# Kernel tuning notes

Measured on AMD Instinct MI355X. Metric: run time of the kernel, lower is better.

The kernel has to match this reference:

```python
import jax, jax.numpy as jnp
import numpy as np

TAU = 2.0      # LIFNode default tau
VTH = 1.0      # v_threshold
ALPHA = 2.0    # ATan surrogate alpha
EPS = 1e-5     # BatchNorm eps
SCALE = 0.125  # hardcoded attention scale
HEADS = 8

@jax.custom_vjp
def atan_spike(x):
    return (x >= 0.0).astype(x.dtype)

def _atan_fwd(x):
    return atan_spike(x), x

def _atan_bwd(x, g):
    sg = (ALPHA / 2.0) / (1.0 + (jnp.pi / 2.0 * ALPHA * x) ** 2)
    return (g * sg,)

atan_spike.defvjp(_atan_fwd, _atan_bwd)

def lif(x_seq):
    # multi-step LIF: v' = v + (x - v)/tau ; spike = H(v'-1) ; hard reset to 0 (detach_reset)
    def step(v, x):
        v = v + (x - v) / TAU
        s = atan_spike(v - VTH)
        v = v * (1.0 - jax.lax.stop_gradient(s))
        return v, s
    _, spikes = jax.lax.scan(step, jnp.zeros_like(x_seq[0]), x_seq)
    return spikes

def bn(x, gamma, beta, mean, var):
    # inference-mode BatchNorm1d over channel axis 2 of [T,B,C,N]
    inv = gamma / jnp.sqrt(var + EPS)
    return x * inv[None, None, :, None] + (beta - mean * inv)[None, None, :, None]

def setup_inputs() -> dict:
    key = jax.random.key(0)
    ks = jax.random.split(key, 24)
    T, B, C, H, W = 4, 8, 512, 32, 32
    inp = {"x": jax.random.normal(ks[0], (T, B, C, H, W), dtype=jnp.float32)}
    i = 1
    for p in ("q", "k", "v", "proj"):
        inp[p + "_w"] = jax.random.normal(ks[i], (C, C), dtype=jnp.float32) / np.sqrt(C); i += 1
        inp[p + "_gamma"] = jax.random.uniform(ks[i], (C,), minval=0.5, maxval=1.5, dtype=jnp.float32); i += 1
        inp[p + "_beta"] = 0.1 * jax.random.normal(ks[i], (C,), dtype=jnp.float32); i += 1
        inp[p + "_mean"] = 0.1 * jax.random.normal(ks[i], (C,), dtype=jnp.float32); i += 1
        inp[p + "_var"] = jax.random.uniform(ks[i], (C,), minval=0.5, maxval=1.5, dtype=jnp.float32); i += 1
    inp["proj_b"] = 0.1 * jax.random.normal(ks[i], (C,), dtype=jnp.float32)
    return inp

def reference(x, q_w, q_gamma, q_beta, q_mean, q_var,
              k_w, k_gamma, k_beta, k_mean, k_var,
              v_w, v_gamma, v_beta, v_mean, v_var,
              proj_w, proj_gamma, proj_beta, proj_mean, proj_var, proj_b):
    T, B, C, H, W = x.shape
    N = H * W
    d = C // HEADS
    s = lif(x).reshape(T, B, C, N)  # proj_lif then flatten HW

    def branch(w, g, b, m, v_):
        y = jnp.einsum('oc,tbcn->tbon', w, s)  # conv1x1 == channel GEMM
        y = lif(bn(y, g, b, m, v_))
        # [T,B,C,N] -> [T,B,h,N,d]
        return y.reshape(T, B, HEADS, d, N).transpose(0, 1, 2, 4, 3)

    q = branch(q_w, q_gamma, q_beta, q_mean, q_var)
    k = branch(k_w, k_gamma, k_beta, k_mean, k_var)
    v = branch(v_w, v_gamma, v_beta, v_mean, v_var)

    kv = jnp.einsum('tbhnd,tbhne->tbhde', k, v)          # k^T v : [T,B,h,d,d]
    att = jnp.einsum('tbhnd,tbhde->tbhne', q, kv) * SCALE  # [T,B,h,N,d]
    att = att.transpose(0, 1, 2, 4, 3).reshape(T, B, C, N)
    a = lif(att)

    y = jnp.einsum('oc,tbcn->tbon', proj_w, a) + proj_b[None, None, :, None]
    y = bn(y, proj_gamma, proj_beta, proj_mean, proj_var)
    return y.reshape(T, B, C, H, W)
```

## Files before the change

kernel.cpp:

```cpp
#include <hip/hip_runtime.h>
#include <cstdint>
#include <cstddef>

typedef unsigned short u16;
typedef __attribute__((ext_vector_type(8))) short sh8;
typedef __attribute__((ext_vector_type(8))) _Float16 hf8;
typedef __attribute__((ext_vector_type(4))) float f4;

#define MFMA16B(a, b, c) __builtin_amdgcn_mfma_f32_16x16x32_bf16((a), (b), (c), 0, 0, 0)
#define MFMA16H(a, b, c) __builtin_amdgcn_mfma_f32_16x16x32_f16((a), (b), (c), 0, 0, 0)

__device__ __forceinline__ u16 f2bf(float f) {
  union { float f; uint32_t u; } v; v.f = f;
  uint32_t u = v.u;
  uint32_t lsb = (u >> 16) & 1u;
  return (u16)((u + 0x7fffu + lsb) >> 16);
}
__device__ __forceinline__ float bf2f(u16 h) {
  union { uint32_t u; float f; } v; v.u = ((uint32_t)h) << 16;
  return v.f;
}

__device__ __forceinline__ void aload16(const void* g, void* l) {
  __builtin_amdgcn_global_load_lds(
      (const __attribute__((address_space(1))) uint32_t*)g,
      (__attribute__((address_space(3))) uint32_t*)l, 16, 0, 0);
}

#define MFMA12(Af, Bf, NB)                                                    \
  {                                                                           \
    __builtin_amdgcn_s_setprio(1);                                            \
    _Pragma("unroll") for (int nf = 0; nf < 2; ++nf)                          \
      _Pragma("unroll") for (int mf = 0; mf < 6; ++mf)                        \
        acc[mf][(NB) + nf] = MFMA16H(Af[mf], Bf[nf], acc[mf][(NB) + nf]);     \
    __builtin_amdgcn_s_setprio(0);                                            \
  }

#define MFMA8(Af, Bf, NB)                                                     \
  {                                                                           \
    __builtin_amdgcn_s_setprio(1);                                            \
    _Pragma("unroll") for (int nf = 0; nf < 2; ++nf)                          \
      _Pragma("unroll") for (int mf = 0; mf < 4; ++mf)                        \
        acc[mf][(NB) + nf] = MFMA16H(Af[mf], Bf[nf], acc[mf][(NB) + nf]);     \
    __builtin_amdgcn_s_setprio(0);                                            \
  }

__global__ void prep_weights(const float* __restrict__ qw, const float* __restrict__ kw,
                             const float* __restrict__ vw, const float* __restrict__ pw,
                             u16* __restrict__ w2qkv, u16* __restrict__ w2p) {
  #pragma clang fp contract(off)
  int row = blockIdx.x;
  for (int c = threadIdx.x; c < 512; c += 256) {
    const float* src;
    if (row < 1536) {
      int br = row >> 9;
      src = (br == 0 ? qw : (br == 1 ? kw : vw)) + (size_t)(row & 511) * 512;
    } else {
      src = pw + (size_t)(row - 1536) * 512;
    }
    float w = src[c];
    _Float16 h0 = (_Float16)w;
    float r1 = w - (float)h0;
    _Float16 h1 = (_Float16)r1;
    union { _Float16 h; u16 u; } u0, u1;
    u0.h = h0; u1.h = h1;
    if (row < 1536) {
      w2qkv[(size_t)row * 1024 + c] = u0.u;
      w2qkv[(size_t)row * 1024 + 512 + c] = u1.u;
    } else {
      int m = row - 1536;
      w2p[(size_t)m * 1024 + c] = u0.u;
      w2p[(size_t)m * 1024 + 512 + c] = u1.u;
    }
  }
}

__global__ void bn_prep(const float* __restrict__ g0, const float* __restrict__ b0,
                        const float* __restrict__ m0, const float* __restrict__ v0,
                        const float* __restrict__ g1, const float* __restrict__ b1,
                        const float* __restrict__ m1, const float* __restrict__ v1,
                        const float* __restrict__ g2, const float* __restrict__ b2,
                        const float* __restrict__ m2, const float* __restrict__ v2,
                        const float* __restrict__ g3, const float* __restrict__ b3,
                        const float* __restrict__ m3, const float* __restrict__ v3,
                        float* __restrict__ inv, float* __restrict__ add) {
  #pragma clang fp contract(off)
  int s = blockIdx.x >> 1;
  int i = (blockIdx.x & 1) * 256 + threadIdx.x;
  const float* g  = s == 0 ? g0 : s == 1 ? g1 : s == 2 ? g2 : g3;
  const float* be = s == 0 ? b0 : s == 1 ? b1 : s == 2 ? b2 : b3;
  const float* mu = s == 0 ? m0 : s == 1 ? m1 : s == 2 ? m2 : m3;
  const float* va = s == 0 ? v0 : s == 1 ? v1 : s == 2 ? v2 : v3;
  float iv = g[i] / sqrtf(va[i] + 1e-5f);
  inv[s * 512 + i] = iv;
  add[s * 512 + i] = be[i] - mu[i] * iv;
}

__global__ __launch_bounds__(256) void lif0(const float* __restrict__ x, u16* __restrict__ sT) {
  #pragma clang fp contract(off)
  __shared__ u16 st[64 * 80];
  const int tid = threadIdx.x;
  const int n0 = blockIdx.x * 64;
  const int c0 = blockIdx.y * 64;
  const int b = blockIdx.z;
  const int cl = tid >> 2;
  const int ns = (tid & 3) * 16;
  const int nr = tid >> 2;
  const int cs = (tid & 3) * 16;
  float vv[16];
#pragma unroll
  for (int i = 0; i < 16; i++) vv[i] = 0.f;
  for (int t = 0; t < 4; ++t) {
    const float* xp = x + ((size_t)((t * 8 + b) * 512 + c0 + cl)) * 1024 + n0 + ns;
#pragma unroll
    for (int q = 0; q < 4; ++q) {
      f4 xv = *(const f4*)(xp + q * 4);
#pragma unroll
      for (int j = 0; j < 4; ++j) {
        int i = q * 4 + j;
        float v2 = vv[i] + (xv[j] - vv[i]) * 0.5f;
        int spk = (v2 - 1.0f >= 0.0f);
        st[(ns + i) * 80 + cl] = spk ? (u16)0x3C00 : (u16)0;
        vv[i] = spk ? 0.0f : v2;
      }
    }
    __syncthreads();
    u16* gp = sT + ((size_t)((t * 8 + b) * 1024 + n0 + nr)) * 512 + c0 + cs;
    *(sh8*)(gp) = *(const sh8*)&st[nr * 80 + cs];
    *(sh8*)(gp + 8) = *(const sh8*)&st[nr * 80 + cs + 8];
    __syncthreads();
  }
}

__global__ __launch_bounds__(512, 2) void qkv_gemm(
    const u16* __restrict__ w2,
    const u16* __restrict__ sT,
    const float* __restrict__ inv4, const float* __restrict__ add4,
    u16* __restrict__ qs, u16* __restrict__ ks, u16* __restrict__ vs) {
  #pragma clang fp contract(off)
  __shared__ u16 lA[2][192 * 64];
  __shared__ u16 lB[3][256 * 64];
  const int tid = threadIdx.x;
  const int bid = blockIdx.x;
  const int orig = (bid & 7) * 32 + (bid >> 3);
  const int mI = orig & 7;
  const int nI = (orig >> 3) & 3;
  const int b  = orig >> 5;
  const int m0 = mI * 192;
  const int n0 = nI * 256;
  const int wid = tid >> 6, lane = tid & 63;
  const int l15 = lane & 15, l4 = lane >> 4;
  const int wm = wid >> 2, wn = wid & 3;
  const int swz = l15 & 7;
  const int srow = tid >> 3;
  const int ss = (tid & 7) ^ (srow & 7);
  int aoff[3];
#pragma unroll
  for (int c = 0; c < 3; ++c)
    aoff[c] = (m0 + c * 64 + srow) * 1024 + (ss >> 2) * 512 + (ss & 3) * 8;
  int boff[4];
#pragma unroll
  for (int c = 0; c < 4; ++c)
    boff[c] = (n0 + c * 64 + srow) * 512 + (ss >> 2) * 32 + (ss & 3) * 8;

  auto stA = [&](int ii) {
    int k0 = (ii & 15) * 32;
    u16* d = &lA[ii & 1][0];
#pragma unroll
    for (int c = 0; c < 3; ++c)
      aload16(w2 + (size_t)(aoff[c] + k0), d + c * 4096 + tid * 8);
  };
  auto stB = [&](int P) {
    int k0 = (P & 7) * 64;
    const u16* bb = sT + (size_t)(P >> 3) * 4194304 + (size_t)b * 524288;
    u16* d = &lB[P % 3][0];
#pragma unroll
    for (int c = 0; c < 4; ++c)
      aload16(bb + (size_t)(boff[c] + k0), d + c * 4096 + tid * 8);
  };

  const f4 fz = {0.f, 0.f, 0.f, 0.f};
  f4 acc[6][4];
  f4 vst[6][4];
#pragma unroll
  for (int i = 0; i < 6; i++)
#pragma unroll
    for (int j = 0; j < 4; j++) vst[i][j] = fz;

  stA(0); stB(0); stB(1);
  asm volatile("s_waitcnt vmcnt(4)" ::: "memory");
  __builtin_amdgcn_s_barrier();
  __builtin_amdgcn_sched_barrier(0);

  for (int t = 0; t < 4; ++t) {
#pragma unroll
    for (int i = 0; i < 6; i++)
#pragma unroll
      for (int j = 0; j < 4; j++) acc[i][j] = fz;

    for (int i = 0; i < 16; ++i) {
      const int ii = t * 16 + i;
      const int P = ii >> 1;
      const u16* bufA = &lA[ii & 1][0];
      const u16* bufB = &lB[P % 3][0];
      const int sb = (ii & 1) * 4;
      const bool issueB = ((ii & 1) == 0) && (P + 2 < 32);
      if (ii < 63) stA(ii + 1);
      if (issueB) stB(P + 2);
      hf8 A0[6], Bq[2];
#pragma unroll
      for (int mf = 0; mf < 6; ++mf) {
        int r = wm * 96 + mf * 16 + l15;
        A0[mf] = *(const hf8*)&bufA[r * 64 + ((l4 ^ swz) * 8)];
      }
#pragma unroll
      for (int nf = 0; nf < 2; ++nf) {
        int r = wn * 64 + nf * 16 + l15;
        Bq[nf] = *(const hf8*)&bufB[r * 64 + (((sb + l4) ^ swz) * 8)];
      }
      MFMA12(A0, Bq, 0);
      hf8 B1[2];
#pragma unroll
      for (int nf = 0; nf < 2; ++nf) {
        int r = wn * 64 + (2 + nf) * 16 + l15;
        B1[nf] = *(const hf8*)&bufB[r * 64 + (((sb + l4) ^ swz) * 8)];
      }
      MFMA12(A0, B1, 2);
      hf8 A1[6];
#pragma unroll
      for (int mf = 0; mf < 6; ++mf) {
        int r = wm * 96 + mf * 16 + l15;
        A1[mf] = *(const hf8*)&bufA[r * 64 + (((4 + l4) ^ swz) * 8)];
      }
      MFMA12(A1, B1, 2);
      MFMA12(A1, Bq, 0);
      if (((ii & 1) == 0) && issueB) {
        asm volatile("s_waitcnt vmcnt(4)" ::: "memory");
      } else {
        asm volatile("s_waitcnt vmcnt(0)" ::: "memory");
      }
      __builtin_amdgcn_s_barrier();
      __builtin_amdgcn_sched_barrier(0);
    }
#pragma unroll
    for (int mf = 0; mf < 6; ++mf) {
      int f0 = m0 + wm * 96 + mf * 16;
      int br = f0 >> 9;
      u16* dst = br == 0 ? qs : (br == 1 ? ks : vs);
      int ocb = f0 & 511;
#pragma unroll
      for (int r = 0; r < 4; ++r) {
        int oc = ocb + l4 * 4 + r;
        float iv = inv4[br * 512 + oc];
        float ad = add4[br * 512 + oc];
        size_t rowbase = ((size_t)((t * 8 + b) * 512 + oc)) * 1024 + n0;
#pragma unroll
        for (int nf = 0; nf < 4; ++nf) {
          float z = acc[mf][nf][r] * iv + ad;
          float v2 = vst[mf][nf][r];
          v2 = v2 + (z - v2) * 0.5f;
          int spk = (v2 - 1.0f >= 0.0f);
          vst[mf][nf][r] = spk ? 0.0f : v2;
          dst[rowbase + wn * 64 + nf * 16 + l15] = spk ? (u16)0x3F80 : (u16)0;
        }
      }
    }
  }
}

__global__ __launch_bounds__(256) void kv_gemm(const u16* __restrict__ ks,
                                               const u16* __restrict__ vs,
                                               float* __restrict__ kvp) {
  const int tbh = blockIdx.x;
  const int tid = threadIdx.x;
  const int wv = tid >> 6, lane = tid & 63, l15 = lane & 15, l4 = lane >> 4;
  const size_t cb = ((size_t)(tbh >> 3) * 512 + (size_t)(tbh & 7) * 64) * 1024;
  const u16* vbase = vs + cb;
  const u16* kbase = ks + cb;
  const f4 fz = {0.f, 0.f, 0.f, 0.f};
  f4 acc[4];
#pragma unroll
  for (int i = 0; i < 4; i++) acc[i] = fz;
  for (int s = 0; s < 32; ++s) {
    int kk = s * 32 + l4 * 8;
    sh8 av = *(const sh8*)(vbase + (size_t)(wv * 16 + l15) * 1024 + kk);
#pragma unroll
    for (int df = 0; df < 4; ++df) {
      sh8 bk = *(const sh8*)(kbase + (size_t)(df * 16 + l15) * 1024 + kk);
      acc[df] = MFMA16B(av, bk, acc[df]);
    }
  }
  float* out = kvp + (size_t)tbh * 4096;
#pragma unroll
  for (int df = 0; df < 4; ++df)
#pragma unroll
    for (int r = 0; r < 4; ++r)
      out[(wv * 16 + l4 * 4 + r) * 64 + df * 16 + l15] = acc[df][r];
}

__global__ __launch_bounds__(256) void att_lif(const u16* __restrict__ qs,
                                               const float* __restrict__ kvp,
                                               u16* __restrict__ aT) {
  #pragma clang fp contract(off)
  __shared__ u16 ldsb[64 * 72 * 2 + 128 * 72];
  u16* lkhi = ldsb;
  u16* lklo = ldsb + 64 * 72;
  u16* lqT = ldsb + 64 * 72 * 2;
  u16* lsp = ldsb;
  const int tid = threadIdx.x;
  const int n0 = blockIdx.x * 128;
  const int b = blockIdx.y >> 3;
  const int h = blockIdx.y & 7;
  const int wv = tid >> 6, lane = tid & 63, l15 = lane & 15, l4 = lane >> 4;
  const int e_s = tid >> 2, ds_ = (tid & 3) * 16;
  const f4 fz = {0.f, 0.f, 0.f, 0.f};
  f4 vst[4][2];
#pragma unroll
  for (int i = 0; i < 4; i++)
#pragma unroll
    for (int j = 0; j < 2; j++) vst[i][j] = fz;

  for (int t = 0; t < 4; ++t) {
    int tb = t * 8 + b;
    int tbh = tb * 8 + h;
    {
      const float* base = kvp + (size_t)tbh * 4096 + e_s * 64 + ds_;
#pragma unroll
      for (int q = 0; q < 4; ++q) {
        f4 s4 = *(const f4*)(base + q * 4);
#pragma unroll
        for (int j = 0; j < 4; ++j) {
          float sv = s4[j];
          u16 hb = f2bf(sv);
          float lof = sv - bf2f(hb);
          lkhi[e_s * 72 + ds_ + q * 4 + j] = hb;
          lklo[e_s * 72 + ds_ + q * 4 + j] = f2bf(lof);
        }
      }
    }
    {
      const u16* qb = qs + ((size_t)tb * 512 + h * 64) * 1024 + n0;
#pragma unroll
      for (int it = 0; it < 4; ++it) {
        int lin = it * 2048 + tid * 8;
        int d = lin >> 7, j0 = lin & 127;
        sh8 qv = *(const sh8*)(qb + (size_t)d * 1024 + j0);
#pragma unroll
        for (int j = 0; j < 8; ++j) lqT[(j0 + j) * 72 + d] = (u16)qv[j];
      }
    }
    __syncthreads();
    f4 acc[4][2];
#pragma unroll
    for (int i = 0; i < 4; i++)
#pragma unroll
      for (int j = 0; j < 2; j++) acc[i][j] = fz;
#pragma unroll
    for (int ksx = 0; ksx < 2; ++ksx) {
      sh8 bq[2];
#pragma unroll
      for (int nf = 0; nf < 2; ++nf)
        bq[nf] = *(const sh8*)&lqT[(wv * 32 + nf * 16 + l15) * 72 + ksx * 32 + l4 * 8];
#pragma unroll
      for (int mf = 0; mf < 4; ++mf) {
        sh8 ah = *(const sh8*)&lkhi[(mf * 16 + l15) * 72 + ksx * 32 + l4 * 8];
        sh8 al = *(const sh8*)&lklo[(mf * 16 + l15) * 72 + ksx * 32 + l4 * 8];
#pragma unroll
        for (int nf = 0; nf < 2; ++nf) {
          acc[mf][nf] = MFMA16B(ah, bq[nf], acc[mf][nf]);
          acc[mf][nf] = MFMA16B(al, bq[nf], acc[mf][nf]);
        }
      }
    }
    __syncthreads();
#pragma unroll
    for (int mf = 0; mf < 4; ++mf)
#pragma unroll
      for (int nf = 0; nf < 2; ++nf)
#pragma unroll
        for (int r = 0; r < 4; ++r) {
          float xatt = acc[mf][nf][r] * 0.125f;
          float v2 = vst[mf][nf][r];
          v2 = v2 + (xatt - v2) * 0.5f;
          int spk = (v2 - 1.0f >= 0.0f);
          vst[mf][nf][r] = spk ? 0.0f : v2;
          int e = mf * 16 + l4 * 4 + r;
          int n = wv * 32 + nf * 16 + l15;
          lsp[n * 72 + e] = spk ? (u16)0x3C00 : (u16)0;
        }
    __syncthreads();
    {
#pragma unroll
      for (int it = 0; it < 2; ++it) {
        int lin = it * 256 + tid;
        int n = lin >> 2, es = (lin & 3) * 16;
        u16* gp = aT + ((size_t)(tb * 1024 + n0 + n)) * 512 + h * 64 + es;
        *(sh8*)gp = *(const sh8*)&lsp[n * 72 + es];
        *(sh8*)(gp + 8) = *(const sh8*)&lsp[n * 72 + es + 8];
      }
    }
    __syncthreads();
  }
}

__global__ __launch_bounds__(512, 2) void proj_gemm(
    const u16* __restrict__ w2,
    const u16* __restrict__ aT,
    const float* __restrict__ inv4, const float* __restrict__ add4,
    const float* __restrict__ pb, float* __restrict__ out) {
  #pragma clang fp contract(off)
  __shared__ u16 lA[2][128 * 64];
  __shared__ u16 lB[3][256 * 64];
  const int tid = threadIdx.x;
  const int bid = blockIdx.x;
  const int orig = (bid & 7) * 64 + (bid >> 3);
  const int mI = orig & 3;
  const int nI = (orig >> 2) & 3;
  const int tb = orig >> 4;
  const int m0 = mI * 128;
  const int n0 = nI * 256;
  const int wid = tid >> 6, lane = tid & 63;
  const int l15 = lane & 15, l4 = lane >> 4;
  const int wm = wid >> 2, wn = wid & 3;
  const int swz = l15 & 7;
  const int srow = tid >> 3;
  const int ss = (tid & 7) ^ (srow & 7);
  int aoff[2];
#pragma unroll
  for (int c = 0; c < 2; ++c)
    aoff[c] = (m0 + c * 64 + srow) * 1024 + (ss >> 2) * 512 + (ss & 3) * 8;
  int boff[4];
#pragma unroll
  for (int c = 0; c < 4; ++c)
    boff[c] = (n0 + c * 64 + srow) * 512 + (ss >> 2) * 32 + (ss & 3) * 8;
  const u16* bb = aT + (size_t)tb * 524288;

  auto stA = [&](int ii) {
    int k0 = (ii & 15) * 32;
    u16* d = &lA[ii & 1][0];
#pragma unroll
    for (int c = 0; c < 2; ++c)
      aload16(w2 + (size_t)(aoff[c] + k0), d + c * 4096 + tid * 8);
  };
  auto stB = [&](int P) {
    int k0 = (P & 7) * 64;
    u16* d = &lB[P % 3][0];
#pragma unroll
    for (int c = 0; c < 4; ++c)
      aload16(bb + (size_t)(boff[c] + k0), d + c * 4096 + tid * 8);
  };

  const f4 fz = {0.f, 0.f, 0.f, 0.f};
  f4 acc[4][4];
#pragma unroll
  for (int i = 0; i < 4; i++)
#pragma unroll
    for (int j = 0; j < 4; j++) acc[i][j] = fz;

  stA(0); stB(0); stB(1);
  asm volatile("s_waitcnt vmcnt(4)" ::: "memory");
  __builtin_amdgcn_s_barrier();
  __builtin_amdgcn_sched_barrier(0);

  for (int ii = 0; ii < 16; ++ii) {
    const int P = ii >> 1;
    const u16* bufA = &lA[ii & 1][0];
    const u16* bufB = &lB[P % 3][0];
    const int sb = (ii & 1) * 4;
    const bool issueB = ((ii & 1) == 0) && (P + 2 < 8);
    if (ii < 15) stA(ii + 1);
    if (issueB) stB(P + 2);
    hf8 A0[4], Bq[2];
#pragma unroll
    for (int mf = 0; mf < 4; ++mf) {
      int r = wm * 64 + mf * 16 + l15;
      A0[mf] = *(const hf8*)&bufA[r * 64 + ((l4 ^ swz) * 8)];
    }
#pragma unroll
    for (int nf = 0; nf < 2; ++nf) {
      int r = wn * 64 + nf * 16 + l15;
      Bq[nf] = *(const hf8*)&bufB[r * 64 + (((sb + l4) ^ swz) * 8)];
    }
    MFMA8(A0, Bq, 0);
    hf8 B1[2];
#pragma unroll
    for (int nf = 0; nf < 2; ++nf) {
      int r = wn * 64 + (2 + nf) * 16 + l15;
      B1[nf] = *(const hf8*)&bufB[r * 64 + (((sb + l4) ^ swz) * 8)];
    }
    MFMA8(A0, B1, 2);
    hf8 A1[4];
#pragma unroll
    for (int mf = 0; mf < 4; ++mf) {
      int r = wm * 64 + mf * 16 + l15;
      A1[mf] = *(const hf8*)&bufA[r * 64 + (((4 + l4) ^ swz) * 8)];
    }
    MFMA8(A1, B1, 2);
    MFMA8(A1, Bq, 0);
    if (((ii & 1) == 0) && issueB) {
      asm volatile("s_waitcnt vmcnt(4)" ::: "memory");
    } else {
      asm volatile("s_waitcnt vmcnt(0)" ::: "memory");
    }
    __builtin_amdgcn_s_barrier();
    __builtin_amdgcn_sched_barrier(0);
  }
#pragma unroll
  for (int mf = 0; mf < 4; ++mf) {
#pragma unroll
    for (int r = 0; r < 4; ++r) {
      int o = m0 + wm * 64 + mf * 16 + l4 * 4 + r;
      float iv = inv4[3 * 512 + o];
      float ad = add4[3 * 512 + o];
      float bias = pb[o];
      size_t rowbase = ((size_t)(tb * 512 + o)) * 1024 + n0;
#pragma unroll
      for (int nf = 0; nf < 4; ++nf) {
        float z = (acc[mf][nf][r] + bias) * iv + ad;
        out[rowbase + wn * 64 + nf * 16 + l15] = z;
      }
    }
  }
}

extern "C" void kernel_launch(void* const* d_in, const int* in_sizes, int n_in,
                              void* d_out, int out_size, void* d_ws, size_t ws_size,
                              hipStream_t stream) {
  const float* x = (const float*)d_in[0];
  const float* qw = (const float*)d_in[1];
  const float* kw = (const float*)d_in[6];
  const float* vw = (const float*)d_in[11];
  const float* pw = (const float*)d_in[16];
  const float* pb = (const float*)d_in[21];

  char* p = (char*)d_ws;
  u16* w2qkv = (u16*)p; p += (size_t)1536 * 1024 * 2;
  u16* w2p = (u16*)p;   p += (size_t)512 * 1024 * 2;
  float* inv4 = (float*)p; p += 4 * 512 * 4;
  float* add4 = (float*)p; p += 4 * 512 * 4;
  u16* sT = (u16*)p;    p += (size_t)4 * 8 * 1024 * 512 * 2;
  u16* qs = (u16*)p;    p += (size_t)4 * 8 * 512 * 1024 * 2;
  u16* ks = (u16*)p;    p += (size_t)4 * 8 * 512 * 1024 * 2;
  u16* vs = (u16*)p;    p += (size_t)4 * 8 * 512 * 1024 * 2;
  float* kvp = (float*)p; p += (size_t)256 * 4096 * 4;
  u16* aT = sT;
  float* out = (float*)d_out;

  prep_weights<<<dim3(2048), dim3(256), 0, stream>>>(qw, kw, vw, pw, w2qkv, w2p);
  bn_prep<<<dim3(8), dim3(256), 0, stream>>>(
      (const float*)d_in[2], (const float*)d_in[3], (const float*)d_in[4], (const float*)d_in[5],
      (const float*)d_in[7], (const float*)d_in[8], (const float*)d_in[9], (const float*)d_in[10],
      (const float*)d_in[12], (const float*)d_in[13], (const float*)d_in[14], (const float*)d_in[15],
      (const float*)d_in[17], (const float*)d_in[18], (const float*)d_in[19], (const float*)d_in[20],
      inv4, add4);
  lif0<<<dim3(16, 8, 8), dim3(256), 0, stream>>>(x, sT);
  qkv_gemm<<<dim3(256), dim3(512), 0, stream>>>(w2qkv, sT, inv4, add4, qs, ks, vs);
  kv_gemm<<<dim3(256), dim3(256), 0, stream>>>(ks, vs, kvp);
  att_lif<<<dim3(8, 64), dim3(256), 0, stream>>>(qs, kvp, aT);
  proj_gemm<<<dim3(512), dim3(512), 0, stream>>>(w2p, aT, inv4, add4, pb, out);
}
```

Baseline: 258.5 us.

## Shrink GEMM tiles to 64-row blocks for higher occupancy in qkv and proj

Both the qkv and projection GEMMs move from large M tiles (192/128 rows) with a triple-buffered B and staggered waits to 64-row M tiles with double-buffered A and B at K step 32. Launch bounds rise to four blocks per CU and grid sizes grow to 768 and 1024 blocks. The aim is more resident waves and better CU coverage so latency is hidden by occupancy instead of deep software pipelining. In exchange each block gets less operand reuse, the same weights and activations are fetched from global memory more often, and every K step now waits on all outstanding loads with vmcnt(0).

```diff
diff --git a/kernel.cpp b/kernel.cpp
--- a/kernel.cpp
+++ b/kernel.cpp
@@ -26,24 +26,6 @@
       (const __attribute__((address_space(1))) uint32_t*)g,
       (__attribute__((address_space(3))) uint32_t*)l, 16, 0, 0);
 }
-
-#define MFMA12(Af, Bf, NB)                                                    \
-  {                                                                           \
-    __builtin_amdgcn_s_setprio(1);                                            \
-    _Pragma("unroll") for (int nf = 0; nf < 2; ++nf)                          \
-      _Pragma("unroll") for (int mf = 0; mf < 6; ++mf)                        \
-        acc[mf][(NB) + nf] = MFMA16H(Af[mf], Bf[nf], acc[mf][(NB) + nf]);     \
-    __builtin_amdgcn_s_setprio(0);                                            \
-  }
-
-#define MFMA8(Af, Bf, NB)                                                     \
-  {                                                                           \
-    __builtin_amdgcn_s_setprio(1);                                            \
-    _Pragma("unroll") for (int nf = 0; nf < 2; ++nf)                          \
-      _Pragma("unroll") for (int mf = 0; mf < 4; ++mf)                        \
-        acc[mf][(NB) + nf] = MFMA16H(Af[mf], Bf[nf], acc[mf][(NB) + nf]);     \
-    __builtin_amdgcn_s_setprio(0);                                            \
-  }
 
 __global__ void prep_weights(const float* __restrict__ qw, const float* __restrict__ kw,
                              const float* __restrict__ vw, const float* __restrict__ pw,
@@ -132,119 +114,104 @@
   }
 }
 
-__global__ __launch_bounds__(512, 2) void qkv_gemm(
+__global__ __launch_bounds__(512, 4) void qkv_gemm(
     const u16* __restrict__ w2,
     const u16* __restrict__ sT,
     const float* __restrict__ inv4, const float* __restrict__ add4,
     u16* __restrict__ qs, u16* __restrict__ ks, u16* __restrict__ vs) {
   #pragma clang fp contract(off)
-  __shared__ u16 lA[2][192 * 64];
-  __shared__ u16 lB[3][256 * 64];
+  __shared__ u16 lA[2][64 * 64];
+  __shared__ u16 lB[2][256 * 32];
   const int tid = threadIdx.x;
   const int bid = blockIdx.x;
-  const int orig = (bid & 7) * 32 + (bid >> 3);
-  const int mI = orig & 7;
-  const int nI = (orig >> 3) & 3;
-  const int b  = orig >> 5;
-  const int m0 = mI * 192;
+  const int orig = (bid & 7) * 96 + (bid >> 3);
+  const int mI = orig % 24;
+  const int rest = orig / 24;
+  const int nI = rest & 3;
+  const int b  = rest >> 2;
+  const int m0 = mI * 64;
   const int n0 = nI * 256;
   const int wid = tid >> 6, lane = tid & 63;
   const int l15 = lane & 15, l4 = lane >> 4;
   const int wm = wid >> 2, wn = wid & 3;
-  const int swz = l15 & 7;
-  const int srow = tid >> 3;
-  const int ss = (tid & 7) ^ (srow & 7);
-  int aoff[3];
-#pragma unroll
-  for (int c = 0; c < 3; ++c)
-    aoff[c] = (m0 + c * 64 + srow) * 1024 + (ss >> 2) * 512 + (ss & 3) * 8;
-  int boff[4];
-#pragma unroll
-  for (int c = 0; c < 4; ++c)
-    boff[c] = (n0 + c * 64 + srow) * 512 + (ss >> 2) * 32 + (ss & 3) * 8;
+  const int swzA = l15 & 7;
+  const int swzB = l15 & 3;
+  const int ssA = (tid & 7) ^ ((tid >> 3) & 7);
+  const int aoff = (m0 + (tid >> 3)) * 1024 + (ssA >> 2) * 512 + (ssA & 3) * 8;
+  const int ssB = (tid & 3) ^ ((tid >> 2) & 3);
+  int boff[2];
+#pragma unroll
+  for (int c = 0; c < 2; ++c)
+    boff[c] = (n0 + c * 128 + (tid >> 2)) * 512 + ssB * 8;
 
   auto stA = [&](int ii) {
     int k0 = (ii & 15) * 32;
-    u16* d = &lA[ii & 1][0];
-#pragma unroll
-    for (int c = 0; c < 3; ++c)
-      aload16(w2 + (size_t)(aoff[c] + k0), d + c * 4096 + tid * 8);
+    aload16(w2 + (size_t)(aoff + k0), &lA[ii & 1][tid * 8]);
   };
-  auto stB = [&](int P) {
-    int k0 = (P & 7) * 64;
-    const u16* bb = sT + (size_t)(P >> 3) * 4194304 + (size_t)b * 524288;
-    u16* d = &lB[P % 3][0];
-#pragma unroll
-    for (int c = 0; c < 4; ++c)
+  auto stB = [&](int ii) {
+    int k0 = (ii & 15) * 32;
+    const u16* bb = sT + (size_t)(ii >> 4) * 4194304 + (size_t)b * 524288;
+    u16* d = &lB[ii & 1][0];
+#pragma unroll
+    for (int c = 0; c < 2; ++c)
       aload16(bb + (size_t)(boff[c] + k0), d + c * 4096 + tid * 8);
   };
 
   const f4 fz = {0.f, 0.f, 0.f, 0.f};
-  f4 acc[6][4];
-  f4 vst[6][4];
-#pragma unroll
-  for (int i = 0; i < 6; i++)
+  f4 acc[2][4];
+  f4 vst[2][4];
+#pragma unroll
+  for (int i = 0; i < 2; i++)
 #pragma unroll
     for (int j = 0; j < 4; j++) vst[i][j] = fz;
 
-  stA(0); stB(0); stB(1);
-  asm volatile("s_waitcnt vmcnt(4)" ::: "memory");
+  stA(0); stB(0);
+  asm volatile("s_waitcnt vmcnt(0)" ::: "memory");
   __builtin_amdgcn_s_barrier();
   __builtin_amdgcn_sched_barrier(0);
 
   for (int t = 0; t < 4; ++t) {
 #pragma unroll
-    for (int i = 0; i < 6; i++)
+    for (int i = 0; i < 2; i++)
 #pragma unroll
       for (int j = 0; j < 4; j++) acc[i][j] = fz;
 
     for (int i = 0; i < 16; ++i) {
       const int ii = t * 16 + i;
-      const int P = ii >> 1;
       const u16* bufA = &lA[ii & 1][0];
-      const u16* bufB = &lB[P % 3][0];
-      const int sb = (ii & 1) * 4;
-      const bool issueB = ((ii & 1) == 0) && (P + 2 < 32);
-      if (ii < 63) stA(ii + 1);
-      if (issueB) stB(P + 2);
-      hf8 A0[6], Bq[2];
-#pragma unroll
-      for (int mf = 0; mf < 6; ++mf) {
-        int r = wm * 96 + mf * 16 + l15;
-        A0[mf] = *(const hf8*)&bufA[r * 64 + ((l4 ^ swz) * 8)];
-      }
-#pragma unroll
-      for (int nf = 0; nf < 2; ++nf) {
+      const u16* bufB = &lB[ii & 1][0];
+      if (ii < 63) { stA(ii + 1); stB(ii + 1); }
+      hf8 A0[2], A1[2], Bf[4];
+#pragma unroll
+      for (int mf = 0; mf < 2; ++mf) {
+        int r = wm * 32 + mf * 16 + l15;
+        A0[mf] = *(const hf8*)&bufA[r * 64 + (((l4) ^ swzA) * 8)];
+        A1[mf] = *(const hf8*)&bufA[r * 64 + (((4 + l4) ^ swzA) * 8)];
+      }
+#pragma unroll
+      for (int nf = 0; nf < 4; ++nf) {
         int r = wn * 64 + nf * 16 + l15;
-        Bq[nf] = *(const hf8*)&bufB[r * 64 + (((sb + l4) ^ swz) * 8)];
-      }
-      MFMA12(A0, Bq, 0);
-      hf8 B1[2];
-#pragma unroll
-      for (int nf = 0; nf < 2; ++nf) {
-        int r = wn * 64 + (2 + nf) * 16 + l15;
-        B1[nf] = *(const hf8*)&bufB[r * 64 + (((sb + l4) ^ swz) * 8)];
-      }
-      MFMA12(A0, B1, 2);
-      hf8 A1[6];
-#pragma unroll
-      for (int mf = 0; mf < 6; ++mf) {
-        int r = wm * 96 + mf * 16 + l15;
-        A1[mf] = *(const hf8*)&bufA[r * 64 + (((4 + l4) ^ swz) * 8)];
-      }
-      MFMA12(A1, B1, 2);
-      MFMA12(A1, Bq, 0);
-      if (((ii & 1) == 0) && issueB) {
-        asm volatile("s_waitcnt vmcnt(4)" ::: "memory");
-      } else {
-        asm volatile("s_waitcnt vmcnt(0)" ::: "memory");
-      }
+        Bf[nf] = *(const hf8*)&bufB[r * 32 + ((l4 ^ swzB) * 8)];
+      }
+      __builtin_amdgcn_s_setprio(1);
+#pragma unroll
+      for (int nf = 0; nf < 4; ++nf)
+#pragma unroll
+        for (int mf = 0; mf < 2; ++mf)
+          acc[mf][nf] = MFMA16H(A0[mf], Bf[nf], acc[mf][nf]);
+#pragma unroll
+      for (int nf = 0; nf < 4; ++nf)
+#pragma unroll
+        for (int mf = 0; mf < 2; ++mf)
+          acc[mf][nf] = MFMA16H(A1[mf], Bf[nf], acc[mf][nf]);
+      __builtin_amdgcn_s_setprio(0);
+      asm volatile("s_waitcnt vmcnt(0)" ::: "memory");
       __builtin_amdgcn_s_barrier();
       __builtin_amdgcn_sched_barrier(0);
     }
 #pragma unroll
-    for (int mf = 0; mf < 6; ++mf) {
-      int f0 = m0 + wm * 96 + mf * 16;
+    for (int mf = 0; mf < 2; ++mf) {
+      int f0 = m0 + wm * 32 + mf * 16;
       int br = f0 >> 9;
       u16* dst = br == 0 ? qs : (br == 1 ? ks : vs);
       int ocb = f0 & 511;
@@ -403,113 +370,97 @@
   }
 }
 
-__global__ __launch_bounds__(512, 2) void proj_gemm(
+__global__ __launch_bounds__(512, 4) void proj_gemm(
     const u16* __restrict__ w2,
     const u16* __restrict__ aT,
     const float* __restrict__ inv4, const float* __restrict__ add4,
     const float* __restrict__ pb, float* __restrict__ out) {
   #pragma clang fp contract(off)
-  __shared__ u16 lA[2][128 * 64];
-  __shared__ u16 lB[3][256 * 64];
+  __shared__ u16 lA[2][64 * 64];
+  __shared__ u16 lB[2][256 * 32];
   const int tid = threadIdx.x;
   const int bid = blockIdx.x;
-  const int orig = (bid & 7) * 64 + (bid >> 3);
-  const int mI = orig & 3;
-  const int nI = (orig >> 2) & 3;
-  const int tb = orig >> 4;
-  const int m0 = mI * 128;
+  const int orig = (bid & 7) * 128 + (bid >> 3);
+  const int mI = orig & 7;
+  const int nI = (orig >> 3) & 3;
+  const int tb = orig >> 5;
+  const int m0 = mI * 64;
   const int n0 = nI * 256;
   const int wid = tid >> 6, lane = tid & 63;
   const int l15 = lane & 15, l4 = lane >> 4;
   const int wm = wid >> 2, wn = wid & 3;
-  const int swz = l15 & 7;
-  const int srow = tid >> 3;
-  const int ss = (tid & 7) ^ (srow & 7);
-  int aoff[2];
+  const int swzA = l15 & 7;
+  const int swzB = l15 & 3;
+  const int ssA = (tid & 7) ^ ((tid >> 3) & 7);
+  const int aoff = (m0 + (tid >> 3)) * 1024 + (ssA >> 2) * 512 + (ssA & 3) * 8;
+  const int ssB = (tid & 3) ^ ((tid >> 2) & 3);
+  int boff[2];
 #pragma unroll
   for (int c = 0; c < 2; ++c)
-    aoff[c] = (m0 + c * 64 + srow) * 1024 + (ss >> 2) * 512 + (ss & 3) * 8;
-  int boff[4];
-#pragma unroll
-  for (int c = 0; c < 4; ++c)
-    boff[c] = (n0 + c * 64 + srow) * 512 + (ss >> 2) * 32 + (ss & 3) * 8;
+    boff[c] = (n0 + c * 128 + (tid >> 2)) * 512 + ssB * 8;
   const u16* bb = aT + (size_t)tb * 524288;
 
   auto stA = [&](int ii) {
     int k0 = (ii & 15) * 32;
-    u16* d = &lA[ii & 1][0];
+    aload16(w2 + (size_t)(aoff + k0), &lA[ii & 1][tid * 8]);
+  };
+  auto stB = [&](int ii) {
+    int k0 = (ii & 15) * 32;
+    u16* d = &lB[ii & 1][0];
 #pragma unroll
     for (int c = 0; c < 2; ++c)
-      aload16(w2 + (size_t)(aoff[c] + k0), d + c * 4096 + tid * 8);
-  };
-  auto stB = [&](int P) {
-    int k0 = (P & 7) * 64;
-    u16* d = &lB[P % 3][0];
-#pragma unroll
-    for (int c = 0; c < 4; ++c)
       aload16(bb + (size_t)(boff[c] + k0), d + c * 4096 + tid * 8);
   };
 
   const f4 fz = {0.f, 0.f, 0.f, 0.f};
-  f4 acc[4][4];
-#pragma unroll
-  for (int i = 0; i < 4; i++)
+  f4 acc[2][4];
+#pragma unroll
+  for (int i = 0; i < 2; i++)
 #pragma unroll
     for (int j = 0; j < 4; j++) acc[i][j] = fz;
 
-  stA(0); stB(0); stB(1);
-  asm volatile("s_waitcnt vmcnt(4)" ::: "memory");
+  stA(0); stB(0);
+  asm volatile("s_waitcnt vmcnt(0)" ::: "memory");
   __builtin_amdgcn_s_barrier();
   __builtin_amdgcn_sched_barrier(0);
 
   for (int ii = 0; ii < 16; ++ii) {
-    const int P = ii >> 1;
     const u16* bufA = &lA[ii & 1][0];
-    const u16* bufB = &lB[P % 3][0];
-    const int sb = (ii & 1) * 4;
-    const bool issueB = ((ii & 1) == 0) && (P + 2 < 8);
-    if (ii < 15) stA(ii + 1);
-    if (issueB) stB(P + 2);
-    hf8 A0[4], Bq[2];
-#pragma unroll
-    for (int mf = 0; mf < 4; ++mf) {
-      int r = wm * 64 + mf * 16 + l15;
-      A0[mf] = *(const hf8*)&bufA[r * 64 + ((l4 ^ swz) * 8)];
-    }
-#pragma unroll
-    for (int nf = 0; nf < 2; ++nf) {
+    const u16* bufB = &lB[ii & 1][0];
+    if (ii < 15) { stA(ii + 1); stB(ii + 1); }
+    hf8 A0[2], A1[2], Bf[4];
+#pragma unroll
+    for (int mf = 0; mf < 2; ++mf) {
+      int r = wm * 32 + mf * 16 + l15;
+      A0[mf] = *(const hf8*)&bufA[r * 64 + (((l4) ^ swzA) * 8)];
+      A1[mf] = *(const hf8*)&bufA[r * 64 + (((4 + l4) ^ swzA) * 8)];
+    }
+#pragma unroll
+    for (int nf = 0; nf < 4; ++nf) {
       int r = wn * 64 + nf * 16 + l15;
-      Bq[nf] = *(const hf8*)&bufB[r * 64 + (((sb + l4) ^ swz) * 8)];
-    }
-    MFMA8(A0, Bq, 0);
-    hf8 B1[2];
-#pragma unroll
-    for (int nf = 0; nf < 2; ++nf) {
-      int r = wn * 64 + (2 + nf) * 16 + l15;
-      B1[nf] = *(const hf8*)&bufB[r * 64 + (((sb + l4) ^ swz) * 8)];
-    }
-    MFMA8(A0, B1, 2);
-    hf8 A1[4];
-#pragma unroll
-    for (int mf = 0; mf < 4; ++mf) {
-      int r = wm * 64 + mf * 16 + l15;
-      A1[mf] = *(const hf8*)&bufA[r * 64 + (((4 + l4) ^ swz) * 8)];
-    }
-    MFMA8(A1, B1, 2);
-    MFMA8(A1, Bq, 0);
-    if (((ii & 1) == 0) && issueB) {
-      asm volatile("s_waitcnt vmcnt(4)" ::: "memory");
-    } else {
-      asm volatile("s_waitcnt vmcnt(0)" ::: "memory");
-    }
+      Bf[nf] = *(const hf8*)&bufB[r * 32 + ((l4 ^ swzB) * 8)];
+    }
+    __builtin_amdgcn_s_setprio(1);
+#pragma unroll
+    for (int nf = 0; nf < 4; ++nf)
+#pragma unroll
+      for (int mf = 0; mf < 2; ++mf)
+        acc[mf][nf] = MFMA16H(A0[mf], Bf[nf], acc[mf][nf]);
+#pragma unroll
+    for (int nf = 0; nf < 4; ++nf)
+#pragma unroll
+      for (int mf = 0; mf < 2; ++mf)
+        acc[mf][nf] = MFMA16H(A1[mf], Bf[nf], acc[mf][nf]);
+    __builtin_amdgcn_s_setprio(0);
+    asm volatile("s_waitcnt vmcnt(0)" ::: "memory");
     __builtin_amdgcn_s_barrier();
     __builtin_amdgcn_sched_barrier(0);
   }
 #pragma unroll
-  for (int mf = 0; mf < 4; ++mf) {
+  for (int mf = 0; mf < 2; ++mf) {
 #pragma unroll
     for (int r = 0; r < 4; ++r) {
-      int o = m0 + wm * 64 + mf * 16 + l4 * 4 + r;
+      int o = m0 + wm * 32 + mf * 16 + l4 * 4 + r;
       float iv = inv4[3 * 512 + o];
       float ad = add4[3 * 512 + o];
       float bias = pb[o];
@@ -554,8 +505,8 @@
       (const float*)d_in[17], (const float*)d_in[18], (const float*)d_in[19], (const float*)d_in[20],
       inv4, add4);
   lif0<<<dim3(16, 8, 8), dim3(256), 0, stream>>>(x, sT);
-  qkv_gemm<<<dim3(256), dim3(512), 0, stream>>>(w2qkv, sT, inv4, add4, qs, ks, vs);
+  qkv_gemm<<<dim3(768), dim3(512), 0, stream>>>(w2qkv, sT, inv4, add4, qs, ks, vs);
   kv_gemm<<<dim3(256), dim3(256), 0, stream>>>(ks, vs, kvp);
   att_lif<<<dim3(8, 64), dim3(256), 0, stream>>>(qs, kvp, aT);
-  proj_gemm<<<dim3(512), dim3(512), 0, stream>>>(w2p, aT, inv4, add4, pb, out);
-}
+  proj_gemm<<<dim3(1024), dim3(512), 0, stream>>>(w2p, aT, inv4, add4, pb, out);
+}
```

New measurement: 297.7 us. 1.15x slower.
